# Kernel tuning notes

Measured on AMD Instinct MI355X. Metric: run time of the kernel, lower is better.

Reference implementation:

```python
import jax, jax.numpy as jnp
import numpy as np
from jax import lax

K = 9      # 3x3 kernel points
PAD = 1
EPS = 1e-5

def _conv3x3(x, w):
    # x: [B,C,H,W], w: [O,C,3,3] -> [B,O,H,W], stride 1, pad 1
    return lax.conv_general_dilated(x, w, (1, 1), [(PAD, PAD), (PAD, PAD)],
                                    dimension_numbers=('NCHW', 'OIHW', 'NCHW'))

def _bilinear_sample(x, py, px):
    # x: [B,C,H,W]; py,px: [B,K,H,W] float sample coords -> [B,C,K,H,W]
    # Zero padding outside bounds (mmcv deform_conv semantics).
    B, C, H, W = x.shape
    y0 = jnp.floor(py)
    x0 = jnp.floor(px)
    wy1 = py - y0
    wx1 = px - x0
    xf = x.reshape(B, C, H * W)

    def corner(yc, xc, wgt):
        valid = (yc >= 0) & (yc <= H - 1) & (xc >= 0) & (xc <= W - 1)
        yi = jnp.clip(yc, 0, H - 1).astype(jnp.int32)
        xi = jnp.clip(xc, 0, W - 1).astype(jnp.int32)
        idx = (yi * W + xi).reshape(B, -1)                       # [B, K*H*W]
        v = jax.vmap(lambda f, i: jnp.take(f, i, axis=1))(xf, idx)  # [B,C,K*H*W]
        v = v.reshape(B, C, K, H, W)
        return v * jnp.where(valid, wgt, 0.0)[:, None]

    return (corner(y0,     x0,     (1 - wy1) * (1 - wx1))
          + corner(y0,     x0 + 1, (1 - wy1) * wx1)
          + corner(y0 + 1, x0,     wy1 * (1 - wx1))
          + corner(y0 + 1, x0 + 1, wy1 * wx1))

def _dcn_bn_relu(x, w_off, b_off, w, gamma, beta, mean, var):
    B, C, H, W = x.shape
    # offset conv: [B, 2K, H, W]; channel pairs are (dy, dx) per kernel point
    off = _conv3x3(x, w_off) + b_off[None, :, None, None]
    off = off.reshape(B, K, 2, H, W)
    dy, dx = off[:, :, 0], off[:, :, 1]
    kk = jnp.arange(K)
    ky = (kk // 3 - PAD).astype(x.dtype)   # kernel y deltas
    kx = (kk % 3 - PAD).astype(x.dtype)    # kernel x deltas
    py = dy + jnp.arange(H, dtype=x.dtype)[None, None, :, None] + ky[None, :, None, None]
    px = dx + jnp.arange(W, dtype=x.dtype)[None, None, None, :] + kx[None, :, None, None]
    s = _bilinear_sample(x, py, px)                       # [B,C,K,H,W]
    out = jnp.einsum('bckhw,ock->bohw', s, w.reshape(w.shape[0], C, K))
    # BatchNorm (eval stats) + ReLU
    inv = gamma * lax.rsqrt(var + EPS)
    return jax.nn.relu(out * inv[None, :, None, None]
                       + (beta - mean * inv)[None, :, None, None])

def setup_inputs() -> dict:
    key = jax.random.key(0)
    ks = jax.random.split(key, 8)
    B, Cin, Cout, H, W = 4, 64, 64, 128, 128
    fan = 1.0 / np.sqrt(Cin * K)
    return {
        'x':      jax.random.normal(ks[0], (B, Cin, H, W), jnp.float32),
        'w_off1': jax.random.normal(ks[1], (2 * K, Cin, 3, 3), jnp.float32) * 0.1,
        'b_off1': jnp.zeros((2 * K,), jnp.float32),
        'w1':     jax.random.normal(ks[2], (Cout, Cin, 3, 3), jnp.float32) * fan,
        'g1':     jnp.ones((Cout,), jnp.float32),
        'be1':    jnp.zeros((Cout,), jnp.float32),
        'm1':     jax.random.normal(ks[3], (Cout,), jnp.float32) * 0.01,
        'v1':     jnp.abs(jax.random.normal(ks[4], (Cout,), jnp.float32)) * 0.1 + 0.9,
        'w_off2': jax.random.normal(ks[5], (2 * K, Cout, 3, 3), jnp.float32) * 0.1,
        'b_off2': jnp.zeros((2 * K,), jnp.float32),
        'w2':     jax.random.normal(ks[6], (Cout, Cout, 3, 3), jnp.float32) * fan,
        'g2':     jnp.ones((Cout,), jnp.float32),
        'be2':    jnp.zeros((Cout,), jnp.float32),
        'm2':     jax.random.normal(ks[7], (Cout,), jnp.float32) * 0.01,
        'v2':     jnp.ones((Cout,), jnp.float32),
    }

def reference(x, w_off1, b_off1, w1, g1, be1, m1, v1,
              w_off2, b_off2, w2, g2, be2, m2, v2):
    h = _dcn_bn_relu(x, w_off1, b_off1, w1, g1, be1, m1, v1)
    return _dcn_bn_relu(h, w_off2, b_off2, w2, g2, be2, m2, v2)
```

## Files before the change

### kernel.cpp

```cpp
#include <hip/hip_runtime.h>

#define BAR_LGKM()                                         \
  do {                                                     \
    asm volatile("s_waitcnt lgkmcnt(0)" ::: "memory");     \
    __builtin_amdgcn_s_barrier();                          \
  } while (0)

__device__ __forceinline__ int swz_block(int bid) {
  return ((bid & 7) << 7) + (bid >> 3);
}


__global__ __launch_bounds__(256) void prep_kernel(
    const float* __restrict__ w1, const float* __restrict__ w2,
    const float* __restrict__ woff1, const float* __restrict__ woff2,
    const float* __restrict__ g1, const float* __restrict__ be1,
    const float* __restrict__ m1, const float* __restrict__ v1,
    const float* __restrict__ g2, const float* __restrict__ be2,
    const float* __restrict__ m2, const float* __restrict__ v2,
    float* __restrict__ ws) {
  float* wt1 = ws;
  float* wt2 = ws + 36864;
  float* wo1 = ws + 73728;
  float* wo2 = ws + 84096;
  float* bn1 = ws + 94464;
  float* bn2 = ws + 94592;
  int idx = blockIdx.x * 256 + threadIdx.x;
  if (idx < 73728) {
    int t = (idx < 36864) ? idx : idx - 36864;
    const float* w = (idx < 36864) ? w1 : w2;
    float* wt = (idx < 36864) ? wt1 : wt2;
    int oi = t & 7;
    int rest = t >> 3;
    int k = rest % 9;
    int cog = rest / 9;
    int og = cog & 7, c = cog >> 3;
    int o = og * 8 + oi;
    wt[t] = w[(o * 64 + c) * 9 + k];
  } else if (idx < 94464) {
    int u = idx - 73728;
    int t2 = (u < 10368) ? u : u - 10368;
    const float* w = (u < 10368) ? woff1 : woff2;
    float* wo = (u < 10368) ? wo1 : wo2;
    int j = t2 % 18;
    int v = t2 / 18;
    int tt = v % 9;
    int c = v / 9;
    wo[t2] = w[(j * 64 + c) * 9 + tt];
  } else if (idx < 94528) {
    int o = idx - 94464;
    float s = g1[o] * rsqrtf(v1[o] + 1e-5f);
    bn1[o] = s;
    bn1[64 + o] = be1[o] - m1[o] * s;
  } else if (idx < 94592) {
    int o = idx - 94528;
    float s = g2[o] * rsqrtf(v2[o] + 1e-5f);
    bn2[o] = s;
    bn2[64 + o] = be2[o] - m2[o] * s;
  }
}

__global__ __launch_bounds__(512, 8) void conv_off_kernel(
    const float* __restrict__ xin, const float* __restrict__ wofft,
    const float* __restrict__ boff, float* __restrict__ off) {
  __shared__ float halo[2][792];
  int tid = threadIdx.x;
  int pxl = tid & 63;
  int og = tid >> 6;
  int ogu = __builtin_amdgcn_readfirstlane(og);
  int p0 = swz_block(blockIdx.x) * 64;
  int b = p0 >> 14, hw0 = p0 & 16383;
  int h = hw0 >> 7, w0 = hw0 & 127;

  bool sv = tid < 396;
  int pp = (tid >= 198) ? 1 : 0;
  int pos = tid - pp * 198;
  int r = pos / 66, cc = pos - r * 66;
  int yy = h + r - 1, xx = w0 + cc - 1;
  bool inb = sv && (yy >= 0) && (yy < 128) && (xx >= 0) && (xx < 128);
  int ofs = (yy << 7) + xx;
  const float* xb0 = xin + ((size_t)(b * 64) << 14);

  float stg0 = inb ? xb0[((size_t)pp << 14) + ofs] : 0.f;
  float stg1 = inb ? xb0[((size_t)(2 + pp) << 14) + ofs] : 0.f;

  int jbase = (ogu < 2) ? ogu * 3 : 6 + (ogu - 2) * 2;
  int nj = (ogu < 2) ? 3 : 2;
  int jc2 = jbase + 2;
  if (jc2 > 17) jc2 = 17;

  float acc[3] = {0.f, 0.f, 0.f};

#pragma unroll 1
  for (int cg = 0; cg < 64; cg += 4) {
    int bufi = (cg >> 2) & 1;
    if (sv) {
      halo[bufi][pp * 198 + pos] = stg0;
      halo[bufi][(2 + pp) * 198 + pos] = stg1;
    }
    if (cg < 60) {
      stg0 = inb ? xb0[((size_t)(cg + 4 + pp) << 14) + ofs] : 0.f;
      stg1 = inb ? xb0[((size_t)(cg + 6 + pp) << 14) + ofs] : 0.f;
    }
    BAR_LGKM();
    const float* hb = halo[bufi];
#pragma unroll
    for (int p = 0; p < 4; ++p) {
      const float* wc = wofft + (cg + p) * 162;
#pragma unroll
      for (int t = 0; t < 9; ++t) {
        float v = hb[p * 198 + (t / 3) * 66 + pxl + (t % 3)];
        acc[0] = fmaf(v, wc[t * 18 + jbase], acc[0]);
        acc[1] = fmaf(v, wc[t * 18 + jbase + 1], acc[1]);
        acc[2] = fmaf(v, wc[t * 18 + jc2], acc[2]);
      }
    }
  }
#pragma unroll
  for (int i = 0; i < 3; ++i) {
    if (i < nj) {
      int j = jbase + i;
      off[((size_t)(b * 18 + j) << 14) + hw0 + pxl] = acc[i] + boff[j];
    }
  }
}

__global__ __launch_bounds__(512, 8) void dcn_main_kernel(
    const float* __restrict__ xin, const float* __restrict__ off,
    const float* __restrict__ wt, const float* __restrict__ bn,
    float* __restrict__ out) {
  __shared__ float prm[576 * 6];
  __shared__ int sortmap[576];
  __shared__ int hist[32];
  __shared__ float sbuf[2][576];
  int tid = threadIdx.x;
  int pxl = tid & 63;
  int og = tid >> 6;
  int ogu = __builtin_amdgcn_readfirstlane(og);
  int p0 = swz_block(blockIdx.x) * 64;
  int b = p0 >> 14, hw0 = p0 & 16383;
  int h = hw0 >> 7, w0 = hw0 & 127;
  const float* xb = xin + ((size_t)b << 20);

  bool act1 = (tid & 7) == 0;
  int s1 = 512 + (tid >> 3);

  if (tid < 32) hist[tid] = 0;

  int bkt[2];
#pragma unroll
  for (int j = 0; j < 2; ++j) {
    bool a = (j == 0) || act1;
    int s = (j == 0) ? tid : s1;
    int k = s >> 6;
    int pxs = s & 63;
    int hw = hw0 + pxs;
    float dy = a ? off[((size_t)(b * 18 + 2 * k) << 14) + hw] : 0.f;
    float dx = a ? off[((size_t)(b * 18 + 2 * k + 1) << 14) + hw] : 0.f;
    float py = (float)(h + k / 3 - 1) + dy;
    float pxf = (float)(w0 + pxs + k % 3 - 1) + dx;
    float y0f = floorf(py), x0f = floorf(pxf);
    float wy1 = py - y0f, wx1 = pxf - x0f;
    float wy0 = 1.f - wy1, wx0 = 1.f - wx1;
    int y0 = (int)y0f, x0 = (int)x0f;
    int y1 = y0 + 1, x1 = x0 + 1;
    bool vy0 = (y0 >= 0) && (y0 <= 127);
    bool vy1 = (y1 >= 0) && (y1 <= 127);
    bool vx0 = (x0 >= 0) && (x0 <= 127);
    bool vx1 = (x1 >= 0) && (x1 <= 127);
    float pw0 = (vy0 && vx0) ? wy0 * wx0 : 0.f;
    float pw1 = (vy0 && vx1) ? wy0 * wx1 : 0.f;
    float pw2 = (vy1 && vx0) ? wy1 * wx0 : 0.f;
    float pw3 = (vy1 && vx1) ? wy1 * wx1 : 0.f;
    int y0c = min(max(y0, 0), 127), y1c = min(max(y1, 0), 127);
    int xb2 = min(max(x0, 0), 126);
    bool se0 = (x0 == xb2);
    bool se1 = (x0 + 1 == xb2);
    float f0 = (se0 ? pw0 : 0.f) + (se1 ? pw1 : 0.f);
    float f1 = (se0 ? 0.f : pw0) + (se1 ? 0.f : pw1);
    float f2 = (se0 ? pw2 : 0.f) + (se1 ? pw3 : 0.f);
    float f3 = (se0 ? 0.f : pw2) + (se1 ? 0.f : pw3);
    if (a) {
      float* pp = &prm[s * 6];
      pp[0] = f0; pp[1] = f1; pp[2] = f2; pp[3] = f3;
      ((int*)pp)[4] = (y0c << 7) + xb2;
      ((int*)pp)[5] = (y1c << 7) + xb2;
    }
    bkt[j] = min(max(y0 - (h - 10), 0), 20);
  }
  __syncthreads();
  atomicAdd(&hist[bkt[0]], 1);
  if (act1) atomicAdd(&hist[bkt[1]], 1);
  __syncthreads();
  if (tid == 0) {
    int run = 0;
#pragma unroll 1
    for (int i = 0; i <= 20; ++i) { int t = hist[i]; hist[i] = run; run += t; }
  }
  __syncthreads();
  {
    int r0 = atomicAdd(&hist[bkt[0]], 1);
    sortmap[r0] = tid;
    if (act1) {
      int r1 = atomicAdd(&hist[bkt[1]], 1);
      sortmap[r1] = s1;
    }
  }
  __syncthreads();

  int ws0 = sortmap[tid];
  int ws1 = act1 ? sortmap[512 + (tid >> 3)] : 0;
  float q[2][4];
  const float* pa[2];
  const float* pb[2];
  {
    const float* pp = &prm[ws0 * 6];
    q[0][0] = pp[0]; q[0][1] = pp[1]; q[0][2] = pp[2]; q[0][3] = pp[3];
    pa[0] = xb + ((const int*)pp)[4];
    pb[0] = xb + ((const int*)pp)[5];
  }
  if (act1) {
    const float* pp = &prm[ws1 * 6];
    q[1][0] = pp[0]; q[1][1] = pp[1]; q[1][2] = pp[2]; q[1][3] = pp[3];
    pa[1] = xb + ((const int*)pp)[4];
    pb[1] = xb + ((const int*)pp)[5];
  } else {
    q[1][0] = q[1][1] = q[1][2] = q[1][3] = 0.f;
    pa[1] = xb; pb[1] = xb;
  }

  float2 t0a = *(const float2*)pa[0];
  float2 t1a = *(const float2*)pb[0];
  float2 t0b = act1 ? *(const float2*)pa[1] : make_float2(0.f, 0.f);
  float2 t1b = act1 ? *(const float2*)pb[1] : make_float2(0.f, 0.f);
  pa[0] += 16384; pb[0] += 16384; pa[1] += 16384; pb[1] += 16384;

  float acc[8];
#pragma unroll
  for (int oi = 0; oi < 8; ++oi) acc[oi] = 0.f;

#pragma unroll 1
  for (int c = 0; c < 64; ++c) {
    sbuf[c & 1][ws0] = fmaf(q[0][0], t0a.x,
                       fmaf(q[0][1], t0a.y,
                       fmaf(q[0][2], t1a.x, q[0][3] * t1a.y)));
    if (act1) {
      sbuf[c & 1][ws1] = fmaf(q[1][0], t0b.x,
                         fmaf(q[1][1], t0b.y,
                         fmaf(q[1][2], t1b.x, q[1][3] * t1b.y)));
    }
    if (c < 63) {
      t0a = *(const float2*)pa[0];
      t1a = *(const float2*)pb[0];
      if (act1) {
        t0b = *(const float2*)pa[1];
        t1b = *(const float2*)pb[1];
      }
      pa[0] += 16384; pb[0] += 16384; pa[1] += 16384; pb[1] += 16384;
    }
    BAR_LGKM();
    const float* wc = wt + (c * 8 + ogu) * 72;
#pragma unroll
    for (int k = 0; k < 9; ++k) {
      float sval = sbuf[c & 1][k * 64 + pxl];
#pragma unroll
      for (int oi = 0; oi < 8; ++oi)
        acc[oi] = fmaf(sval, wc[k * 8 + oi], acc[oi]);
    }
  }

#pragma unroll
  for (int oi = 0; oi < 8; ++oi) {
    int o = ogu * 8 + oi;
    float rres = fmaf(acc[oi], bn[o], bn[64 + o]);
    out[((size_t)(b * 64 + o) << 14) + hw0 + pxl] = fmaxf(rres, 0.f);
  }
}

extern "C" void kernel_launch(void* const* d_in, const int* in_sizes, int n_in,
                              void* d_out, int out_size, void* d_ws, size_t ws_size,
                              hipStream_t stream) {
  const float* x      = (const float*)d_in[0];
  const float* w_off1 = (const float*)d_in[1];
  const float* b_off1 = (const float*)d_in[2];
  const float* w1     = (const float*)d_in[3];
  const float* g1     = (const float*)d_in[4];
  const float* be1    = (const float*)d_in[5];
  const float* m1     = (const float*)d_in[6];
  const float* v1     = (const float*)d_in[7];
  const float* w_off2 = (const float*)d_in[8];
  const float* b_off2 = (const float*)d_in[9];
  const float* w2     = (const float*)d_in[10];
  const float* g2     = (const float*)d_in[11];
  const float* be2    = (const float*)d_in[12];
  const float* m2     = (const float*)d_in[13];
  const float* v2     = (const float*)d_in[14];
  float* out = (float*)d_out;

  float* ws   = (float*)d_ws;
  float* wt1  = ws;
  float* wt2  = ws + 36864;
  float* wo1  = ws + 73728;
  float* wo2  = ws + 84096;
  float* bn1  = ws + 94464;
  float* bn2  = ws + 94592;
  float* offb = ws + 94720;
  float* hbuf = ws + 1274368;

  prep_kernel<<<370, 256, 0, stream>>>(w1, w2, w_off1, w_off2,
                                       g1, be1, m1, v1, g2, be2, m2, v2, ws);

  conv_off_kernel<<<1024, 512, 0, stream>>>(x, wo1, b_off1, offb);
  dcn_main_kernel<<<1024, 512, 0, stream>>>(x, offb, wt1, bn1, hbuf);

  conv_off_kernel<<<1024, 512, 0, stream>>>(hbuf, wo2, b_off2, offb);
  dcn_main_kernel<<<1024, 512, 0, stream>>>(hbuf, offb, wt2, bn2, out);
}
```

Baseline: 335.8 us.

## Retile offset conv to full image rows and vectorize sampled-value LDS reads

The offset-conv kernel now gives each block a full 128-pixel row with 4 output groups of 4-5 offset channels, instead of 64-pixel strips with 8 groups of 2-3 channels. This halves the grid and lowers the halo overhead per output. The DCN main kernel stores sampled values pixel-major with a stride of 12, so each thread loads its 9 kernel-point values with two float4 reads plus one scalar instead of nine scalar LDS reads. Costs are more registers per thread in the offset conv, fewer blocks in flight, and possible LDS bank conflicts from the strided scatter writes.

```diff
diff --git a/kernel.cpp b/kernel.cpp
--- a/kernel.cpp
+++ b/kernel.cpp
@@ -63,64 +63,78 @@
 __global__ __launch_bounds__(512, 8) void conv_off_kernel(
     const float* __restrict__ xin, const float* __restrict__ wofft,
     const float* __restrict__ boff, float* __restrict__ off) {
-  __shared__ float halo[2][792];
+  __shared__ float halo[2][1560];
   int tid = threadIdx.x;
-  int pxl = tid & 63;
-  int og = tid >> 6;
+  int px = tid & 127;
+  int og = tid >> 7;
   int ogu = __builtin_amdgcn_readfirstlane(og);
-  int p0 = swz_block(blockIdx.x) * 64;
-  int b = p0 >> 14, hw0 = p0 & 16383;
-  int h = hw0 >> 7, w0 = hw0 & 127;
-
-  bool sv = tid < 396;
-  int pp = (tid >= 198) ? 1 : 0;
-  int pos = tid - pp * 198;
-  int r = pos / 66, cc = pos - r * 66;
-  int yy = h + r - 1, xx = w0 + cc - 1;
-  bool inb = sv && (yy >= 0) && (yy < 128) && (xx >= 0) && (xx < 128);
-  int ofs = (yy << 7) + xx;
+  int rid = ((blockIdx.x & 7) << 6) + (blockIdx.x >> 3);
+  int b = rid >> 7, h = rid & 127;
   const float* xb0 = xin + ((size_t)(b * 64) << 14);
 
-  float stg0 = inb ? xb0[((size_t)pp << 14) + ofs] : 0.f;
-  float stg1 = inb ? xb0[((size_t)(2 + pp) << 14) + ofs] : 0.f;
-
-  int jbase = (ogu < 2) ? ogu * 3 : 6 + (ogu - 2) * 2;
-  int nj = (ogu < 2) ? 3 : 2;
-  int jc2 = jbase + 2;
-  if (jc2 > 17) jc2 = 17;
-
-  float acc[3] = {0.f, 0.f, 0.f};
+  int sofs[4]; int spl[4]; bool svld[4], sok[4];
+#pragma unroll
+  for (int i = 0; i < 4; ++i) {
+    int e = tid + (i << 9);
+    bool ok = e < 1560;
+    int ec = ok ? e : 0;
+    int p = ec / 390;
+    int rr = ec - p * 390;
+    int r = rr / 130;
+    int cc = rr - r * 130;
+    int y = h + r - 1, xx = cc - 1;
+    sok[i] = ok;
+    svld[i] = ok && (y >= 0) && (y < 128) && (xx >= 0) && (xx < 128);
+    sofs[i] = (y << 7) + xx;
+    spl[i] = p;
+  }
+
+  float stg[4];
+#pragma unroll
+  for (int i = 0; i < 4; ++i)
+    stg[i] = svld[i] ? xb0[((size_t)spl[i] << 14) + sofs[i]] : 0.f;
+
+  int jbase = (ogu < 2) ? ogu * 5 : 10 + (ogu - 2) * 4;
+  int nj = (ogu < 2) ? 5 : 4;
+  int j4 = jbase + 4;
+  if (j4 > 17) j4 = 17;
+
+  float acc[5] = {0.f, 0.f, 0.f, 0.f, 0.f};
 
 #pragma unroll 1
   for (int cg = 0; cg < 64; cg += 4) {
     int bufi = (cg >> 2) & 1;
-    if (sv) {
-      halo[bufi][pp * 198 + pos] = stg0;
-      halo[bufi][(2 + pp) * 198 + pos] = stg1;
-    }
+#pragma unroll
+    for (int i = 0; i < 4; ++i)
+      if (sok[i]) halo[bufi][tid + (i << 9)] = stg[i];
     if (cg < 60) {
-      stg0 = inb ? xb0[((size_t)(cg + 4 + pp) << 14) + ofs] : 0.f;
-      stg1 = inb ? xb0[((size_t)(cg + 6 + pp) << 14) + ofs] : 0.f;
+#pragma unroll
+      for (int i = 0; i < 4; ++i)
+        stg[i] = svld[i] ? xb0[((size_t)(cg + 4 + spl[i]) << 14) + sofs[i]]
+                         : 0.f;
     }
     BAR_LGKM();
     const float* hb = halo[bufi];
 #pragma unroll
     for (int p = 0; p < 4; ++p) {
       const float* wc = wofft + (cg + p) * 162;
+      const float* base = hb + p * 390 + px;
 #pragma unroll
       for (int t = 0; t < 9; ++t) {
-        float v = hb[p * 198 + (t / 3) * 66 + pxl + (t % 3)];
+        float v = base[(t / 3) * 130 + (t % 3)];
         acc[0] = fmaf(v, wc[t * 18 + jbase], acc[0]);
         acc[1] = fmaf(v, wc[t * 18 + jbase + 1], acc[1]);
-        acc[2] = fmaf(v, wc[t * 18 + jc2], acc[2]);
+        acc[2] = fmaf(v, wc[t * 18 + jbase + 2], acc[2]);
+        acc[3] = fmaf(v, wc[t * 18 + jbase + 3], acc[3]);
+        acc[4] = fmaf(v, wc[t * 18 + j4], acc[4]);
       }
     }
   }
 #pragma unroll
-  for (int i = 0; i < 3; ++i) {
+  for (int i = 0; i < 5; ++i) {
     if (i < nj) {
       int j = jbase + i;
-      off[((size_t)(b * 18 + j) << 14) + hw0 + pxl] = acc[i] + boff[j];
+      off[((size_t)(b * 18 + j) << 14) + (h << 7) + px] = acc[i] + boff[j];
     }
   }
 }
@@ -132,7 +146,7 @@
   __shared__ float prm[576 * 6];
   __shared__ int sortmap[576];
   __shared__ int hist[32];
-  __shared__ float sbuf[2][576];
+  __shared__ __align__(16) float sbuf[2][768];
   int tid = threadIdx.x;
   int pxl = tid & 63;
   int og = tid >> 6;
@@ -210,6 +224,8 @@
 
   int ws0 = sortmap[tid];
   int ws1 = act1 ? sortmap[512 + (tid >> 3)] : 0;
+  int wsa0 = (ws0 & 63) * 12 + (ws0 >> 6);
+  int wsa1 = (ws1 & 63) * 12 + (ws1 >> 6);
   float q[2][4];
   const float* pa[2];
   const float* pb[2];
@@ -241,13 +257,13 @@
 
 #pragma unroll 1
   for (int c = 0; c < 64; ++c) {
-    sbuf[c & 1][ws0] = fmaf(q[0][0], t0a.x,
-                       fmaf(q[0][1], t0a.y,
-                       fmaf(q[0][2], t1a.x, q[0][3] * t1a.y)));
+    sbuf[c & 1][wsa0] = fmaf(q[0][0], t0a.x,
+                        fmaf(q[0][1], t0a.y,
+                        fmaf(q[0][2], t1a.x, q[0][3] * t1a.y)));
     if (act1) {
-      sbuf[c & 1][ws1] = fmaf(q[1][0], t0b.x,
-                         fmaf(q[1][1], t0b.y,
-                         fmaf(q[1][2], t1b.x, q[1][3] * t1b.y)));
+      sbuf[c & 1][wsa1] = fmaf(q[1][0], t0b.x,
+                          fmaf(q[1][1], t0b.y,
+                          fmaf(q[1][2], t1b.x, q[1][3] * t1b.y)));
     }
     if (c < 63) {
       t0a = *(const float2*)pa[0];
@@ -260,12 +276,16 @@
     }
     BAR_LGKM();
     const float* wc = wt + (c * 8 + ogu) * 72;
+    const float* sb = &sbuf[c & 1][pxl * 12];
+    float4 sA = *(const float4*)sb;
+    float4 sB = *(const float4*)(sb + 4);
+    float s8 = sb[8];
+    float sv[9] = {sA.x, sA.y, sA.z, sA.w, sB.x, sB.y, sB.z, sB.w, s8};
 #pragma unroll
     for (int k = 0; k < 9; ++k) {
-      float sval = sbuf[c & 1][k * 64 + pxl];
 #pragma unroll
       for (int oi = 0; oi < 8; ++oi)
-        acc[oi] = fmaf(sval, wc[k * 8 + oi], acc[oi]);
+        acc[oi] = fmaf(sv[k], wc[k * 8 + oi], acc[oi]);
     }
   }
 
@@ -310,9 +330,9 @@
   prep_kernel<<<370, 256, 0, stream>>>(w1, w2, w_off1, w_off2,
                                        g1, be1, m1, v1, g2, be2, m2, v2, ws);
 
-  conv_off_kernel<<<1024, 512, 0, stream>>>(x, wo1, b_off1, offb);
+  conv_off_kernel<<<512, 512, 0, stream>>>(x, wo1, b_off1, offb);
   dcn_main_kernel<<<1024, 512, 0, stream>>>(x, offb, wt1, bn1, hbuf);
 
-  conv_off_kernel<<<1024, 512, 0, stream>>>(hbuf, wo2, b_off2, offb);
+  conv_off_kernel<<<512, 512, 0, stream>>>(hbuf, wo2, b_off2, offb);
   dcn_main_kernel<<<1024, 512, 0, stream>>>(hbuf, offb, wt2, bn2, out);
 }
```

After: 327.8 us. 1.02x faster.
